# Kernel optimization log

Measured on AMD Instinct MI355X. Metric: run time of the kernel, lower is better.

## Reference

```python
import jax, jax.numpy as jnp
import numpy as np

B, N, S, VOCAB, D, NNZ = 16, 2048, 4096, 50257, 128, 1048576


def setup_inputs() -> dict:
    key = jax.random.key(0)
    k1, k2, k3, k4, k5, k6 = jax.random.split(key, 6)
    return {
        "subnode_ids": jax.random.randint(k1, (B, S), 0, VOCAB),
        "mask_batch": jax.random.randint(k2, (NNZ,), 0, B),
        "mask_node": jax.random.randint(k3, (NNZ,), 0, N),
        "mask_subnode": jax.random.randint(k4, (NNZ,), 0, S),
        "mask_values": jax.random.uniform(k5, (NNZ,), dtype=jnp.float32),
        "emb_table": jax.random.normal(k6, (VOCAB, D), dtype=jnp.float32),
    }


def reference(subnode_ids, mask_batch, mask_node, mask_subnode, mask_values, emb_table):
    # Gather token embeddings for every (batch, subnode) slot: [B, S, D] -> [B*S, D]
    subnode_emb = emb_table[subnode_ids].reshape(B * S, D)
    # Flattened COO indices (same as batch*max_nodes + node, batch*max_subnodes + subnode)
    row = mask_batch * N + mask_node      # destination node slot in [0, B*N)
    col = mask_batch * S + mask_subnode   # source subnode slot in [0, B*S)
    # Fused gather + weighted scatter-add (== sparse.mm of expanded_mask @ subnode_emb)
    contrib = subnode_emb[col] * mask_values[:, None]           # [NNZ, D]
    pooled = jax.ops.segment_sum(contrib, row, num_segments=B * N)  # [B*N, D]
    return pooled.reshape(B, N, D)
```

## Files before the change

kernel.cpp:

```cpp
#include <hip/hip_runtime.h>
#include <hip/hip_fp16.h>

#define Bq 16
#define Nq 2048
#define Sq 4096
#define Dq 128
#define VOCABq 50257
#define NNZq 1048576
#define ROWS (Bq * Nq)
#define NBIN 512
#define RPB 64
#define TPB 512
#define BEPT 4
#define ENT (TPB * BEPT)
#define NBLK (NNZq / ENT)
#define NKEY 256
#define EBUF 2560
#define NQUAD ((VOCABq * Dq) / 4)

typedef unsigned long long u64;
typedef u64 u64x2 __attribute__((ext_vector_type(2)));
typedef float vfloat4 __attribute__((ext_vector_type(4)));
typedef unsigned short vushort4 __attribute__((ext_vector_type(4)));
typedef unsigned short vushort8 __attribute__((ext_vector_type(8)));

__device__ __forceinline__ int scan_block(int val, int t, int* waveSum) {
    int lane = t & 63, wid = t >> 6;
    int vi = val;
    #pragma unroll
    for (int d = 1; d < 64; d <<= 1) {
        int w = __shfl_up(vi, d, 64);
        if (lane >= d) vi += w;
    }
    if (lane == 63) waveSum[wid] = vi;
    __syncthreads();
    if (t == 0) {
        int s = 0;
        #pragma unroll
        for (int w = 0; w < TPB / 64; w++) { int x = waveSum[w]; waveSum[w] = s; s += x; }
    }
    __syncthreads();
    return vi - val + waveSum[wid];
}

__device__ __forceinline__ void accum_range(
    const u64* ebuf, int s0, int s1, int lane16,
    const unsigned short* __restrict__ emb16, vfloat4& A0, vfloat4& A1)
{
    int k = s0;
    for (; k + 8 <= s1; k += 8) {
        int tk[8]; float vv[8];
        #pragma unroll
        for (int u = 0; u < 8; u++) {
            u64 pk = ebuf[k + u];
            tk[u] = (int)(pk & 0xFFFF);
            vv[u] = __int_as_float((int)(pk >> 32));
        }
        vushort8 e[8];
        #pragma unroll
        for (int u = 0; u < 8; u++)
            e[u] = reinterpret_cast<const vushort8*>(emb16 + (size_t)tk[u] * Dq)[lane16];
        #pragma unroll
        for (int u = 0; u < 8; u++) {
            A0.x += __half2float(__ushort_as_half(e[u][0])) * vv[u];
            A0.y += __half2float(__ushort_as_half(e[u][1])) * vv[u];
            A0.z += __half2float(__ushort_as_half(e[u][2])) * vv[u];
            A0.w += __half2float(__ushort_as_half(e[u][3])) * vv[u];
            A1.x += __half2float(__ushort_as_half(e[u][4])) * vv[u];
            A1.y += __half2float(__ushort_as_half(e[u][5])) * vv[u];
            A1.z += __half2float(__ushort_as_half(e[u][6])) * vv[u];
            A1.w += __half2float(__ushort_as_half(e[u][7])) * vv[u];
        }
    }
    for (; k < s1; k++) {
        u64 pk = ebuf[k];
        int   tok = (int)(pk & 0xFFFF);
        float v2  = __int_as_float((int)(pk >> 32));
        vushort8 e = reinterpret_cast<const vushort8*>(emb16 + (size_t)tok * Dq)[lane16];
        A0.x += __half2float(__ushort_as_half(e[0])) * v2;
        A0.y += __half2float(__ushort_as_half(e[1])) * v2;
        A0.z += __half2float(__ushort_as_half(e[2])) * v2;
        A0.w += __half2float(__ushort_as_half(e[3])) * v2;
        A1.x += __half2float(__ushort_as_half(e[4])) * v2;
        A1.y += __half2float(__ushort_as_half(e[5])) * v2;
        A1.z += __half2float(__ushort_as_half(e[6])) * v2;
        A1.w += __half2float(__ushort_as_half(e[7])) * v2;
    }
}

__global__ __launch_bounds__(256) void cast_kernel(
    const float* __restrict__ emb, unsigned short* __restrict__ emb16)
{
    int i = blockIdx.x * 256 + threadIdx.x;
    if (i >= NQUAD) return;
    vfloat4 f = reinterpret_cast<const vfloat4*>(emb)[i];
    vushort4 h;
    h.x = __half_as_ushort(__float2half_rn(f.x));
    h.y = __half_as_ushort(__float2half_rn(f.y));
    h.z = __half_as_ushort(__float2half_rn(f.z));
    h.w = __half_as_ushort(__float2half_rn(f.w));
    __builtin_nontemporal_store(h, reinterpret_cast<vushort4*>(emb16) + i);
}

__global__ __launch_bounds__(TPB) void bin_kernel(
    const int* __restrict__ subnode_ids,
    const int* __restrict__ mb,
    const int* __restrict__ mn,
    const int* __restrict__ ms,
    const float* __restrict__ mv,
    u64* __restrict__ binMem,
    unsigned* __restrict__ offTab)
{
    __shared__ int hist[NBIN];
    __shared__ int lstart[NBIN];
    __shared__ int waveSum[TPB / 64];
    __shared__ u64 spk[ENT] __attribute__((aligned(16)));

    int t   = threadIdx.x;
    int blk = blockIdx.x;

    hist[t] = 0;
    __syncthreads();

    int base = blk * ENT;
    int g[BEPT], rank[BEPT];
    u64 pk[BEPT];
    #pragma unroll
    for (int k = 0; k < BEPT; k++) {
        int i   = base + k * TPB + t;
        int b   = __builtin_nontemporal_load(mb + i);
        int row = b * Nq + __builtin_nontemporal_load(mn + i);
        int s   = __builtin_nontemporal_load(ms + i);
        float v = __builtin_nontemporal_load(mv + i);
        int tok = subnode_ids[b * Sq + s];
        g[k]  = row >> 6;
        pk[k] = ((u64)(unsigned)__float_as_int(v) << 32)
              | ((u64)(row & 63) << 16)
              | (unsigned)tok;
        rank[k] = atomicAdd(&hist[g[k]], 1);
    }
    __syncthreads();

    int cnt = hist[t];
    int ex  = scan_block(cnt, t, waveSum);
    lstart[t] = ex;
    offTab[blk * NBIN + t] = (unsigned)ex | ((unsigned)cnt << 16);
    __syncthreads();

    #pragma unroll
    for (int k = 0; k < BEPT; k++)
        spk[lstart[g[k]] + rank[k]] = pk[k];
    __syncthreads();

    const u64x2* s2 = reinterpret_cast<const u64x2*>(spk);
    u64x2* d2 = reinterpret_cast<u64x2*>(binMem + (size_t)blk * ENT);
    #pragma unroll
    for (int p = t; p < ENT / 2; p += TPB) d2[p] = s2[p];
}

__global__ __launch_bounds__(TPB) void pool_kernel(
    const unsigned short* __restrict__ emb16,
    const u64* __restrict__ binMem,
    const unsigned* __restrict__ offTab,
    float* __restrict__ out)
{
    __shared__ u64 spk[EBUF] __attribute__((aligned(16)));
    __shared__ u64 ebuf[EBUF];
    __shared__ int waveSum[TPB / 64];
    __shared__ int khist[NKEY];
    __shared__ int kstart[NKEY + 1];
    __shared__ int kcursor[NKEY];
    __shared__ int nTot;

    int t   = threadIdx.x;
    int bin = blockIdx.x;

    unsigned m = offTab[t * NBIN + bin];
    int soff = (int)(m & 0xFFFFu);
    int scnt = (int)(m >> 16);
    int db   = scan_block(scnt, t, waveSum);
    if (t == TPB - 1) nTot = db + scnt;
    if (db >= EBUF) scnt = 0;
    else if (db + scnt > EBUF) scnt = EBUF - db;

    {
        const u64* src = binMem + (size_t)t * ENT + soff;
        for (int i = 0; i < scnt; i++) spk[db + i] = src[i];
    }
    if (t < NKEY) khist[t] = 0;
    __syncthreads();

    int n = nTot < EBUF ? nTot : EBUF;

    for (int e = t; e < n; e += TPB) {
        u64 p = spk[e];
        int key = (((int)(p & 0xFFFF)) >> 14 << 6) | ((int)(p >> 16) & 63);
        atomicAdd(&khist[key], 1);
    }
    __syncthreads();

    int kval = (t < NKEY) ? khist[t] : 0;
    int kex  = scan_block(kval, t, waveSum);
    if (t < NKEY) {
        kstart[t]  = kex;
        kcursor[t] = kex;
        if (t == NKEY - 1) kstart[NKEY] = kex + kval;
    }
    __syncthreads();

    for (int e = t; e < n; e += TPB) {
        u64 p = spk[e];
        int key = (((int)(p & 0xFFFF)) >> 14 << 6) | ((int)(p >> 16) & 63);
        int pos = atomicAdd(&kcursor[key], 1);
        ebuf[pos] = p;
    }
    __syncthreads();

    int g2     = t >> 4;
    int lane16 = t & 15;
    int r0 = g2, r1 = g2 + 32;
    vfloat4 a0 = {0.f,0.f,0.f,0.f}, a1 = {0.f,0.f,0.f,0.f};
    vfloat4 b0 = {0.f,0.f,0.f,0.f}, b1 = {0.f,0.f,0.f,0.f};
    #pragma unroll
    for (int q = 0; q < 4; q++) {
        accum_range(ebuf, kstart[q * 64 + r0], kstart[q * 64 + r0 + 1], lane16, emb16, a0, a1);
        accum_range(ebuf, kstart[q * 64 + r1], kstart[q * 64 + r1 + 1], lane16, emb16, b0, b1);
    }

    float* orow0 = out + ((size_t)bin * RPB + r0) * Dq + lane16 * 8;
    float* orow1 = out + ((size_t)bin * RPB + r1) * Dq + lane16 * 8;
    __builtin_nontemporal_store(a0, reinterpret_cast<vfloat4*>(orow0));
    __builtin_nontemporal_store(a1, reinterpret_cast<vfloat4*>(orow0) + 1);
    __builtin_nontemporal_store(b0, reinterpret_cast<vfloat4*>(orow1));
    __builtin_nontemporal_store(b1, reinterpret_cast<vfloat4*>(orow1) + 1);
}

extern "C" void kernel_launch(void* const* d_in, const int* in_sizes, int n_in,
                              void* d_out, int out_size, void* d_ws, size_t ws_size,
                              hipStream_t stream) {
    const int*   subnode_ids  = (const int*)d_in[0];
    const int*   mask_batch   = (const int*)d_in[1];
    const int*   mask_node    = (const int*)d_in[2];
    const int*   mask_subnode = (const int*)d_in[3];
    const float* mask_values  = (const float*)d_in[4];
    const float* emb_table    = (const float*)d_in[5];
    float*       out          = (float*)d_out;

    unsigned short* emb16 = (unsigned short*)d_ws;
    u64* binMem = (u64*)(emb16 + (size_t)VOCABq * Dq + 64 );
    unsigned* offTab = (unsigned*)(binMem + (size_t)NBLK * ENT);

    cast_kernel<<<(NQUAD + 255) / 256, 256, 0, stream>>>(emb_table, emb16);
    bin_kernel<<<NBLK, TPB, 0, stream>>>(
        subnode_ids, mask_batch, mask_node, mask_subnode, mask_values,
        binMem, offTab);
    pool_kernel<<<NBIN, TPB, 0, stream>>>(emb16, binMem, offTab, out);
}
```

Before: 135.8 us.

## Enlarge bin blocks, split slice copies across thread pairs, interleave paired row gathers

The bin kernel now uses 1024-thread blocks of 4096 entries each, which halves the number of blocks and gives the pool kernel 256 slices. In the pool kernel, each slice's copy into shared memory is split between two threads. Accumulation now issues 16 embedding gathers at once for the two rows a thread owns, and the scalar tail is replaced by a predicated 8-wide tail. The aim is more memory-level parallelism in the gather phase and less per-block overhead. In exchange, register pressure rises and the bin kernel has a larger shared footprint.

```diff
diff --git a/kernel.cpp b/kernel.cpp
--- a/kernel.cpp
+++ b/kernel.cpp
@@ -10,10 +10,11 @@
 #define ROWS (Bq * Nq)
 #define NBIN 512
 #define RPB 64
-#define TPB 512
+#define BTPB 1024
 #define BEPT 4
-#define ENT (TPB * BEPT)
+#define ENT (BTPB * BEPT)
 #define NBLK (NNZq / ENT)
+#define PTPB 512
 #define NKEY 256
 #define EBUF 2560
 #define NQUAD ((VOCABq * Dq) / 4)
@@ -24,6 +25,7 @@
 typedef unsigned short vushort4 __attribute__((ext_vector_type(4)));
 typedef unsigned short vushort8 __attribute__((ext_vector_type(8)));
 
+template <int NW>
 __device__ __forceinline__ int scan_block(int val, int t, int* waveSum) {
     int lane = t & 63, wid = t >> 6;
     int vi = val;
@@ -37,17 +39,26 @@
     if (t == 0) {
         int s = 0;
         #pragma unroll
-        for (int w = 0; w < TPB / 64; w++) { int x = waveSum[w]; waveSum[w] = s; s += x; }
+        for (int w = 0; w < NW; w++) { int x = waveSum[w]; waveSum[w] = s; s += x; }
     }
     __syncthreads();
     return vi - val + waveSum[wid];
 }
 
+#define FMA8(e_, v_, A0_, A1_)                                   \
+    A0_.x += __half2float(__ushort_as_half(e_[0])) * v_;         \
+    A0_.y += __half2float(__ushort_as_half(e_[1])) * v_;         \
+    A0_.z += __half2float(__ushort_as_half(e_[2])) * v_;         \
+    A0_.w += __half2float(__ushort_as_half(e_[3])) * v_;         \
+    A1_.x += __half2float(__ushort_as_half(e_[4])) * v_;         \
+    A1_.y += __half2float(__ushort_as_half(e_[5])) * v_;         \
+    A1_.z += __half2float(__ushort_as_half(e_[6])) * v_;         \
+    A1_.w += __half2float(__ushort_as_half(e_[7])) * v_;
+
 __device__ __forceinline__ void accum_range(
-    const u64* ebuf, int s0, int s1, int lane16,
+    const u64* ebuf, int k, int s1, int lane16,
     const unsigned short* __restrict__ emb16, vfloat4& A0, vfloat4& A1)
 {
-    int k = s0;
     for (; k + 8 <= s1; k += 8) {
         int tk[8]; float vv[8];
         #pragma unroll
@@ -61,31 +72,53 @@
         for (int u = 0; u < 8; u++)
             e[u] = reinterpret_cast<const vushort8*>(emb16 + (size_t)tk[u] * Dq)[lane16];
         #pragma unroll
+        for (int u = 0; u < 8; u++) { FMA8(e[u], vv[u], A0, A1) }
+    }
+    int rem = s1 - k;
+    if (rem > 0) {
+        int tk[8]; float vv[8]; vushort8 e[8];
+        #pragma unroll
+        for (int u = 0; u < 8; u++) if (u < rem) {
+            u64 pk = ebuf[k + u];
+            tk[u] = (int)(pk & 0xFFFF);
+            vv[u] = __int_as_float((int)(pk >> 32));
+        }
+        #pragma unroll
+        for (int u = 0; u < 8; u++) if (u < rem)
+            e[u] = reinterpret_cast<const vushort8*>(emb16 + (size_t)tk[u] * Dq)[lane16];
+        #pragma unroll
+        for (int u = 0; u < 8; u++) if (u < rem) { FMA8(e[u], vv[u], A0, A1) }
+    }
+}
+
+__device__ __forceinline__ void accum_pair(
+    const u64* ebuf, int ka, int s1a, int kb, int s1b, int lane16,
+    const unsigned short* __restrict__ emb16,
+    vfloat4& A0, vfloat4& A1, vfloat4& B0, vfloat4& B1)
+{
+    while (ka + 8 <= s1a && kb + 8 <= s1b) {
+        int tk[16]; float vv[16];
+        #pragma unroll
         for (int u = 0; u < 8; u++) {
-            A0.x += __half2float(__ushort_as_half(e[u][0])) * vv[u];
-            A0.y += __half2float(__ushort_as_half(e[u][1])) * vv[u];
-            A0.z += __half2float(__ushort_as_half(e[u][2])) * vv[u];
-            A0.w += __half2float(__ushort_as_half(e[u][3])) * vv[u];
-            A1.x += __half2float(__ushort_as_half(e[u][4])) * vv[u];
-            A1.y += __half2float(__ushort_as_half(e[u][5])) * vv[u];
-            A1.z += __half2float(__ushort_as_half(e[u][6])) * vv[u];
-            A1.w += __half2float(__ushort_as_half(e[u][7])) * vv[u];
+            u64 pa = ebuf[ka + u];
+            tk[u]     = (int)(pa & 0xFFFF);
+            vv[u]     = __int_as_float((int)(pa >> 32));
+            u64 pb = ebuf[kb + u];
+            tk[u + 8] = (int)(pb & 0xFFFF);
+            vv[u + 8] = __int_as_float((int)(pb >> 32));
         }
-    }
-    for (; k < s1; k++) {
-        u64 pk = ebuf[k];
-        int   tok = (int)(pk & 0xFFFF);
-        float v2  = __int_as_float((int)(pk >> 32));
-        vushort8 e = reinterpret_cast<const vushort8*>(emb16 + (size_t)tok * Dq)[lane16];
-        A0.x += __half2float(__ushort_as_half(e[0])) * v2;
-        A0.y += __half2float(__ushort_as_half(e[1])) * v2;
-        A0.z += __half2float(__ushort_as_half(e[2])) * v2;
-        A0.w += __half2float(__ushort_as_half(e[3])) * v2;
-        A1.x += __half2float(__ushort_as_half(e[4])) * v2;
-        A1.y += __half2float(__ushort_as_half(e[5])) * v2;
-        A1.z += __half2float(__ushort_as_half(e[6])) * v2;
-        A1.w += __half2float(__ushort_as_half(e[7])) * v2;
-    }
+        vushort8 e[16];
+        #pragma unroll
+        for (int u = 0; u < 16; u++)
+            e[u] = reinterpret_cast<const vushort8*>(emb16 + (size_t)tk[u] * Dq)[lane16];
+        #pragma unroll
+        for (int u = 0; u < 8; u++) { FMA8(e[u], vv[u], A0, A1) }
+        #pragma unroll
+        for (int u = 0; u < 8; u++) { FMA8(e[u + 8], vv[u + 8], B0, B1) }
+        ka += 8; kb += 8;
+    }
+    accum_range(ebuf, ka, s1a, lane16, emb16, A0, A1);
+    accum_range(ebuf, kb, s1b, lane16, emb16, B0, B1);
 }
 
 __global__ __launch_bounds__(256) void cast_kernel(
@@ -102,7 +135,7 @@
     __builtin_nontemporal_store(h, reinterpret_cast<vushort4*>(emb16) + i);
 }
 
-__global__ __launch_bounds__(TPB) void bin_kernel(
+__global__ __launch_bounds__(BTPB) void bin_kernel(
     const int* __restrict__ subnode_ids,
     const int* __restrict__ mb,
     const int* __restrict__ mn,
@@ -113,13 +146,13 @@
 {
     __shared__ int hist[NBIN];
     __shared__ int lstart[NBIN];
-    __shared__ int waveSum[TPB / 64];
+    __shared__ int waveSum[BTPB / 64];
     __shared__ u64 spk[ENT] __attribute__((aligned(16)));
 
     int t   = threadIdx.x;
     int blk = blockIdx.x;
 
-    hist[t] = 0;
+    if (t < NBIN) hist[t] = 0;
     __syncthreads();
 
     int base = blk * ENT;
@@ -127,7 +160,7 @@
     u64 pk[BEPT];
     #pragma unroll
     for (int k = 0; k < BEPT; k++) {
-        int i   = base + k * TPB + t;
+        int i   = base + k * BTPB + t;
         int b   = __builtin_nontemporal_load(mb + i);
         int row = b * Nq + __builtin_nontemporal_load(mn + i);
         int s   = __builtin_nontemporal_load(ms + i);
@@ -141,10 +174,12 @@
     }
     __syncthreads();
 
-    int cnt = hist[t];
-    int ex  = scan_block(cnt, t, waveSum);
-    lstart[t] = ex;
-    offTab[blk * NBIN + t] = (unsigned)ex | ((unsigned)cnt << 16);
+    int cnt = (t < NBIN) ? hist[t] : 0;
+    int ex  = scan_block<BTPB / 64>(cnt, t, waveSum);
+    if (t < NBIN) {
+        lstart[t] = ex;
+        offTab[blk * NBIN + t] = (unsigned)ex | ((unsigned)cnt << 16);
+    }
     __syncthreads();
 
     #pragma unroll
@@ -155,10 +190,10 @@
     const u64x2* s2 = reinterpret_cast<const u64x2*>(spk);
     u64x2* d2 = reinterpret_cast<u64x2*>(binMem + (size_t)blk * ENT);
     #pragma unroll
-    for (int p = t; p < ENT / 2; p += TPB) d2[p] = s2[p];
-}
-
-__global__ __launch_bounds__(TPB) void pool_kernel(
+    for (int p = t; p < ENT / 2; p += BTPB) d2[p] = s2[p];
+}
+
+__global__ __launch_bounds__(PTPB) void pool_kernel(
     const unsigned short* __restrict__ emb16,
     const u64* __restrict__ binMem,
     const unsigned* __restrict__ offTab,
@@ -166,7 +201,7 @@
 {
     __shared__ u64 spk[EBUF] __attribute__((aligned(16)));
     __shared__ u64 ebuf[EBUF];
-    __shared__ int waveSum[TPB / 64];
+    __shared__ int waveSum[PTPB / 64];
     __shared__ int khist[NKEY];
     __shared__ int kstart[NKEY + 1];
     __shared__ int kcursor[NKEY];
@@ -175,24 +210,28 @@
     int t   = threadIdx.x;
     int bin = blockIdx.x;
 
-    unsigned m = offTab[t * NBIN + bin];
+    int slice = t >> 1, half = t & 1;
+    unsigned m = offTab[slice * NBIN + bin];
     int soff = (int)(m & 0xFFFFu);
-    int scnt = (int)(m >> 16);
-    int db   = scan_block(scnt, t, waveSum);
-    if (t == TPB - 1) nTot = db + scnt;
-    if (db >= EBUF) scnt = 0;
-    else if (db + scnt > EBUF) scnt = EBUF - db;
+    int c    = (int)(m >> 16);
+    int c0   = (c + 1) >> 1;
+    int myoff = soff + (half ? c0 : 0);
+    int myc   = half ? (c - c0) : c0;
+    int db = scan_block<PTPB / 64>(myc, t, waveSum);
+    if (t == PTPB - 1) nTot = db + myc;
+    if (db >= EBUF) myc = 0;
+    else if (db + myc > EBUF) myc = EBUF - db;
 
     {
-        const u64* src = binMem + (size_t)t * ENT + soff;
-        for (int i = 0; i < scnt; i++) spk[db + i] = src[i];
+        const u64* src = binMem + (size_t)slice * ENT + myoff;
+        for (int i = 0; i < myc; i++) spk[db + i] = src[i];
     }
     if (t < NKEY) khist[t] = 0;
     __syncthreads();
 
     int n = nTot < EBUF ? nTot : EBUF;
 
-    for (int e = t; e < n; e += TPB) {
+    for (int e = t; e < n; e += PTPB) {
         u64 p = spk[e];
         int key = (((int)(p & 0xFFFF)) >> 14 << 6) | ((int)(p >> 16) & 63);
         atomicAdd(&khist[key], 1);
@@ -200,7 +239,7 @@
     __syncthreads();
 
     int kval = (t < NKEY) ? khist[t] : 0;
-    int kex  = scan_block(kval, t, waveSum);
+    int kex  = scan_block<PTPB / 64>(kval, t, waveSum);
     if (t < NKEY) {
         kstart[t]  = kex;
         kcursor[t] = kex;
@@ -208,7 +247,7 @@
     }
     __syncthreads();
 
-    for (int e = t; e < n; e += TPB) {
+    for (int e = t; e < n; e += PTPB) {
         u64 p = spk[e];
         int key = (((int)(p & 0xFFFF)) >> 14 << 6) | ((int)(p >> 16) & 63);
         int pos = atomicAdd(&kcursor[key], 1);
@@ -223,8 +262,10 @@
     vfloat4 b0 = {0.f,0.f,0.f,0.f}, b1 = {0.f,0.f,0.f,0.f};
     #pragma unroll
     for (int q = 0; q < 4; q++) {
-        accum_range(ebuf, kstart[q * 64 + r0], kstart[q * 64 + r0 + 1], lane16, emb16, a0, a1);
-        accum_range(ebuf, kstart[q * 64 + r1], kstart[q * 64 + r1 + 1], lane16, emb16, b0, b1);
+        accum_pair(ebuf,
+                   kstart[q * 64 + r0], kstart[q * 64 + r0 + 1],
+                   kstart[q * 64 + r1], kstart[q * 64 + r1 + 1],
+                   lane16, emb16, a0, a1, b0, b1);
     }
 
     float* orow0 = out + ((size_t)bin * RPB + r0) * Dq + lane16 * 8;
@@ -251,8 +292,8 @@
     unsigned* offTab = (unsigned*)(binMem + (size_t)NBLK * ENT);
 
     cast_kernel<<<(NQUAD + 255) / 256, 256, 0, stream>>>(emb_table, emb16);
-    bin_kernel<<<NBLK, TPB, 0, stream>>>(
+    bin_kernel<<<NBLK, BTPB, 0, stream>>>(
         subnode_ids, mask_batch, mask_node, mask_subnode, mask_values,
         binMem, offTab);
-    pool_kernel<<<NBIN, TPB, 0, stream>>>(emb16, binMem, offTab, out);
-}
+    pool_kernel<<<NBIN, PTPB, 0, stream>>>(emb16, binMem, offTab, out);
+}
```

New measurement: 133.4 us. About the same (-1.8%).
